# Kernel optimization log

Hardware: AMD Instinct MI355X
Metric: run time of the kernel (lower is better)

## Reference

```python
import jax, jax.numpy as jnp
import numpy as np

N_NODES = 50000
N_EDGES = 400000
IN_DIM = 128
HID_DIM = 128
OUT_DIM = 128


def setup_inputs() -> dict:
    key = jax.random.key(0)
    k_x, k_e, k_w1, k_b1, k_w2, k_b2 = jax.random.split(key, 6)
    x = jax.random.normal(k_x, (N_NODES, IN_DIM), dtype=jnp.float32)
    edge_index = jax.random.randint(k_e, (2, N_EDGES), 0, N_NODES, dtype=jnp.int64)
    # nn.Linear-style params: W is [out, in], kaiming-uniform-ish init
    lim1 = 1.0 / np.sqrt(IN_DIM)
    lim2 = 1.0 / np.sqrt(HID_DIM)
    W1 = jax.random.uniform(k_w1, (HID_DIM, IN_DIM), jnp.float32, -lim1, lim1)
    b1 = jax.random.uniform(k_b1, (HID_DIM,), jnp.float32, -lim1, lim1)
    W2 = jax.random.uniform(k_w2, (OUT_DIM, HID_DIM), jnp.float32, -lim2, lim2)
    b2 = jax.random.uniform(k_b2, (OUT_DIM,), jnp.float32, -lim2, lim2)
    return {"x": x, "edge_index": edge_index, "W1": W1, "b1": b1, "W2": W2, "b2": b2}


def reference(x, edge_index, W1, b1, W2, b2):
    # h = relu(fc1(x));  dropout in eval mode -> identity
    h = jax.nn.relu(x @ W1.T + b1)                      # [N, hid]
    src, dst = edge_index[0], edge_index[1]
    # gather messages from src, scatter-add (mean) into dst
    agg = jax.ops.segment_sum(h[src], dst, num_segments=N_NODES)      # [N, hid]
    deg = jax.ops.segment_sum(jnp.ones_like(dst, dtype=h.dtype), dst,
                              num_segments=N_NODES)                   # [N]
    deg = jnp.maximum(deg, 1.0)
    agg = agg / deg[:, None]
    # residual add + fc2
    return (agg + h) @ W2.T + b2                        # [N, out]
```

## Files before the change

kernel.cpp:

```cpp
#include <hip/hip_runtime.h>

#define N_NODES 50000
#define N_EDGES 400000
#define DIM 128
#define N_SCAN_BLK ((N_NODES + 255) / 256)
#define BUCKET_BLK ((N_EDGES + 255) / 256)
#define FC1_BLK ((N_NODES + 63) / 64)
#define AGG_BLK (N_NODES / 16)

typedef unsigned short u16;
typedef unsigned int   u32;
typedef __bf16 v8bf  __attribute__((ext_vector_type(8)));
typedef float  f32x4 __attribute__((ext_vector_type(4)));
typedef u16    u16x8 __attribute__((ext_vector_type(8)));

union BF8 { u16x8 u; v8bf b; };

__device__ __forceinline__ float bf2f(u16 u) {
    union { u32 i; float f; } v; v.i = ((u32)u) << 16; return v.f;
}
__device__ __forceinline__ u16 f2bf(float f) {
    union { float f; u32 i; } v; v.f = f; u32 u = v.i;
    return (u16)((u + 0x7FFFu + ((u >> 16) & 1u)) >> 16);
}

__global__ __launch_bounds__(256, 3) void count_fc1_kernel(
    const int* __restrict__ esrc, const int* __restrict__ edst,
    int* __restrict__ counts, int* __restrict__ occ,
    const float* __restrict__ x, const float* __restrict__ W1,
    const float* __restrict__ b1, u16* __restrict__ h)
{
    __shared__ u16 xs[64 * 136];
    const int bid = blockIdx.x;

    if (bid < BUCKET_BLK) {
        int e = bid * 256 + threadIdx.x;
        if (e < N_EDGES) {
            int src = esrc[e], dst = edst[e];
            if ((unsigned)src < N_NODES && (unsigned)dst < N_NODES)
                occ[e] = atomicAdd(&counts[dst], 1);
        }
        return;
    }

    const int t = threadIdx.x;
    const int wave = t >> 6, lane = t & 63, quad = lane >> 4, l15 = lane & 15;
    const int ch = wave >> 1, rh = wave & 1;
    const int row0 = (bid - BUCKET_BLK) * 64;

    BF8 barr[4][4];
#pragma unroll
    for (int ct = 0; ct < 4; ++ct)
#pragma unroll
        for (int ks = 0; ks < 4; ++ks) {
            const float* wp = W1 + (size_t)(ch * 64 + ct * 16 + l15) * DIM
                                 + ks * 32 + quad * 8;
            float4 f0 = *(const float4*)wp;
            float4 f1 = *(const float4*)(wp + 4);
            u16x8 p;
            p[0] = f2bf(f0.x); p[1] = f2bf(f0.y); p[2] = f2bf(f0.z); p[3] = f2bf(f0.w);
            p[4] = f2bf(f1.x); p[5] = f2bf(f1.y); p[6] = f2bf(f1.z); p[7] = f2bf(f1.w);
            barr[ct][ks].u = p;
        }

    {
        int srow = t >> 2, k0 = (t & 3) * 32;
        int grow = row0 + srow; if (grow >= N_NODES) grow = N_NODES - 1;
        const float* xp = x + (size_t)grow * DIM + k0;
#pragma unroll
        for (int j = 0; j < 4; ++j) {
            float4 f0 = *(const float4*)(xp + j * 8);
            float4 f1 = *(const float4*)(xp + j * 8 + 4);
            u16x8 p;
            p[0] = f2bf(f0.x); p[1] = f2bf(f0.y); p[2] = f2bf(f0.z); p[3] = f2bf(f0.w);
            p[4] = f2bf(f1.x); p[5] = f2bf(f1.y); p[6] = f2bf(f1.z); p[7] = f2bf(f1.w);
            *(u16x8*)&xs[srow * 136 + k0 + j * 8] = p;
        }
    }

    f32x4 acc[2][4];
#pragma unroll
    for (int ct = 0; ct < 4; ++ct) {
        float bv = b1[ch * 64 + ct * 16 + l15];
        acc[0][ct] = (f32x4){bv, bv, bv, bv};
        acc[1][ct] = (f32x4){bv, bv, bv, bv};
    }
    __syncthreads();

#pragma unroll
    for (int ks = 0; ks < 4; ++ks) {
        BF8 a0, a1;
        a0.u = *(const u16x8*)&xs[(rh * 32 +  0 + l15) * 136 + ks * 32 + quad * 8];
        a1.u = *(const u16x8*)&xs[(rh * 32 + 16 + l15) * 136 + ks * 32 + quad * 8];
#pragma unroll
        for (int ct = 0; ct < 4; ++ct) {
            acc[0][ct] = __builtin_amdgcn_mfma_f32_16x16x32_bf16(
                a0.b, barr[ct][ks].b, acc[0][ct], 0, 0, 0);
            acc[1][ct] = __builtin_amdgcn_mfma_f32_16x16x32_bf16(
                a1.b, barr[ct][ks].b, acc[1][ct], 0, 0, 0);
        }
    }

#pragma unroll
    for (int rt = 0; rt < 2; ++rt)
#pragma unroll
        for (int i = 0; i < 4; ++i) {
            int row = row0 + rh * 32 + rt * 16 + quad * 4 + i;
            if (row < N_NODES) {
#pragma unroll
                for (int ct = 0; ct < 4; ++ct) {
                    int col = ch * 64 + ct * 16 + l15;
                    h[(size_t)row * DIM + col] = f2bf(fmaxf(acc[rt][ct][i], 0.f));
                }
            }
        }
}

__global__ __launch_bounds__(256) void scan_ticket_kernel(
    const int* __restrict__ counts, int* __restrict__ row_ptr,
    int* __restrict__ gcursor)
{
    __shared__ int tmp[256];
    __shared__ int sbase;
    const int t = threadIdx.x;
    const int i = blockIdx.x * 256 + t;
    int v = (i < N_NODES) ? counts[i] : 0;
    tmp[t] = v;
    __syncthreads();
#pragma unroll
    for (int ofs = 1; ofs < 256; ofs <<= 1) {
        int add = (t >= ofs) ? tmp[t - ofs] : 0;
        __syncthreads();
        tmp[t] += add;
        __syncthreads();
    }
    if (t == 255) sbase = atomicAdd(gcursor, tmp[255]);
    __syncthreads();
    if (i < N_NODES) row_ptr[i] = sbase + tmp[t] - v;
}

__global__ __launch_bounds__(256) void scatter_kernel(
    const int* __restrict__ esrc, const int* __restrict__ edst,
    const int* __restrict__ occ, const int* __restrict__ row_ptr,
    int* __restrict__ esorted)
{
    int e = blockIdx.x * 256 + threadIdx.x;
    if (e >= N_EDGES) return;
    int src = esrc[e], dst = edst[e];
    if ((unsigned)src < N_NODES && (unsigned)dst < N_NODES)
        esorted[row_ptr[dst] + occ[e]] = src;
}

__global__ __launch_bounds__(256) void agg_fc2_kernel(
    const int* __restrict__ row_ptr, const int* __restrict__ counts,
    const int* __restrict__ esorted, const u16* __restrict__ h,
    const float* __restrict__ W2, const float* __restrict__ b2,
    float* __restrict__ out)
{
    __shared__ u16 xs[16 * 136];
    const int t = threadIdx.x;
    const int wv = t >> 6, lane = t & 63, quad = lane >> 4, l15 = lane & 15;
    const int row0 = blockIdx.x * 16;

    {
        const int s = wv * 4 + quad;
        const int n = row0 + s;
        const int start = row_ptr[n];
        const int deg   = counts[n];
        const int end   = start + deg;

        u16x8 hres = *(const u16x8*)(h + (size_t)n * DIM + l15 * 8);

        float a[8];
#pragma unroll
        for (int j = 0; j < 8; ++j) a[j] = 0.f;

        int e = start;
        for (; e + 8 <= end; e += 8) {
            int s0 = esorted[e + 0], s1 = esorted[e + 1];
            int s2 = esorted[e + 2], s3 = esorted[e + 3];
            int s4 = esorted[e + 4], s5 = esorted[e + 5];
            int s6 = esorted[e + 6], s7 = esorted[e + 7];
            u16x8 v0 = *(const u16x8*)(h + (size_t)s0 * DIM + l15 * 8);
            u16x8 v1 = *(const u16x8*)(h + (size_t)s1 * DIM + l15 * 8);
            u16x8 v2 = *(const u16x8*)(h + (size_t)s2 * DIM + l15 * 8);
            u16x8 v3 = *(const u16x8*)(h + (size_t)s3 * DIM + l15 * 8);
            u16x8 v4 = *(const u16x8*)(h + (size_t)s4 * DIM + l15 * 8);
            u16x8 v5 = *(const u16x8*)(h + (size_t)s5 * DIM + l15 * 8);
            u16x8 v6 = *(const u16x8*)(h + (size_t)s6 * DIM + l15 * 8);
            u16x8 v7 = *(const u16x8*)(h + (size_t)s7 * DIM + l15 * 8);
#pragma unroll
            for (int j = 0; j < 8; ++j) {
                a[j] += bf2f(v0[j]); a[j] += bf2f(v1[j]);
                a[j] += bf2f(v2[j]); a[j] += bf2f(v3[j]);
                a[j] += bf2f(v4[j]); a[j] += bf2f(v5[j]);
                a[j] += bf2f(v6[j]); a[j] += bf2f(v7[j]);
            }
        }
        for (; e + 4 <= end; e += 4) {
            int s0 = esorted[e + 0], s1 = esorted[e + 1];
            int s2 = esorted[e + 2], s3 = esorted[e + 3];
            u16x8 v0 = *(const u16x8*)(h + (size_t)s0 * DIM + l15 * 8);
            u16x8 v1 = *(const u16x8*)(h + (size_t)s1 * DIM + l15 * 8);
            u16x8 v2 = *(const u16x8*)(h + (size_t)s2 * DIM + l15 * 8);
            u16x8 v3 = *(const u16x8*)(h + (size_t)s3 * DIM + l15 * 8);
#pragma unroll
            for (int j = 0; j < 8; ++j) {
                a[j] += bf2f(v0[j]); a[j] += bf2f(v1[j]);
                a[j] += bf2f(v2[j]); a[j] += bf2f(v3[j]);
            }
        }
        for (; e < end; ++e) {
            u16x8 v = *(const u16x8*)(h + (size_t)esorted[e] * DIM + l15 * 8);
#pragma unroll
            for (int j = 0; j < 8; ++j) a[j] += bf2f(v[j]);
        }

        float inv = (deg > 0) ? 1.f / (float)deg : 1.f;
        u16x8 pk;
#pragma unroll
        for (int j = 0; j < 8; ++j)
            pk[j] = f2bf(a[j] * inv + bf2f(hres[j]));
        *(u16x8*)&xs[s * 136 + l15 * 8] = pk;
    }

    BF8 barr[2][4];
#pragma unroll
    for (int ct = 0; ct < 2; ++ct)
#pragma unroll
        for (int ks = 0; ks < 4; ++ks) {
            const float* wp = W2 + (size_t)(wv * 32 + ct * 16 + l15) * DIM
                                 + ks * 32 + quad * 8;
            float4 f0 = *(const float4*)wp;
            float4 f1 = *(const float4*)(wp + 4);
            u16x8 p;
            p[0] = f2bf(f0.x); p[1] = f2bf(f0.y); p[2] = f2bf(f0.z); p[3] = f2bf(f0.w);
            p[4] = f2bf(f1.x); p[5] = f2bf(f1.y); p[6] = f2bf(f1.z); p[7] = f2bf(f1.w);
            barr[ct][ks].u = p;
        }

    f32x4 acc[2];
#pragma unroll
    for (int ct = 0; ct < 2; ++ct) {
        float bv = b2[wv * 32 + ct * 16 + l15];
        acc[ct] = (f32x4){bv, bv, bv, bv};
    }
    __syncthreads();

#pragma unroll
    for (int ks = 0; ks < 4; ++ks) {
        BF8 a0;
        a0.u = *(const u16x8*)&xs[l15 * 136 + ks * 32 + quad * 8];
#pragma unroll
        for (int ct = 0; ct < 2; ++ct) {
            acc[ct] = __builtin_amdgcn_mfma_f32_16x16x32_bf16(
                a0.b, barr[ct][ks].b, acc[ct], 0, 0, 0);
        }
    }

#pragma unroll
    for (int i = 0; i < 4; ++i) {
        int row = row0 + quad * 4 + i;
#pragma unroll
        for (int ct = 0; ct < 2; ++ct) {
            int col = wv * 32 + ct * 16 + l15;
            out[(size_t)row * DIM + col] = acc[ct][i];
        }
    }
}

extern "C" void kernel_launch(void* const* d_in, const int* in_sizes, int n_in,
                              void* d_out, int out_size, void* d_ws, size_t ws_size,
                              hipStream_t stream)
{
    const float* x  = (const float*)d_in[0];
    const int*   ei = (const int*)d_in[1];
    const float* W1 = (const float*)d_in[2];
    const float* b1 = (const float*)d_in[3];
    const float* W2 = (const float*)d_in[4];
    const float* b2 = (const float*)d_in[5];
    float* out = (float*)d_out;

    const int* esrc = ei;
    const int* edst = ei + N_EDGES;

    char* ws = (char*)d_ws;
    size_t off = 0;
    u16* h       = (u16*)(ws + off); off += (size_t)N_NODES * DIM * 2;
    int* counts  = (int*)(ws + off); off += (size_t)N_NODES * 4;
    int* gcursor = (int*)(ws + off); off += 4;
    int* row_ptr = (int*)(ws + off); off += (size_t)N_NODES * 4;
    int* occ     = (int*)(ws + off); off += (size_t)N_EDGES * 4;
    int* esorted = (int*)(ws + off); off += (size_t)N_EDGES * 4;

    hipMemsetAsync(counts, 0, (size_t)(N_NODES + 1) * 4, stream);

    count_fc1_kernel<<<BUCKET_BLK + FC1_BLK, 256, 0, stream>>>(
        esrc, edst, counts, occ, x, W1, b1, h);
    scan_ticket_kernel<<<N_SCAN_BLK, 256, 0, stream>>>(
        counts, row_ptr, gcursor);
    scatter_kernel<<<BUCKET_BLK, 256, 0, stream>>>(
        esrc, edst, occ, row_ptr, esorted);
    agg_fc2_kernel<<<AGG_BLK, 256, 0, stream>>>(
        row_ptr, counts, esorted, h, W2, b2, out);
}
```

Before: 175.7 us.

## Pad CSR rows to multiples of four, vectorize edge kernels, precast W2

The scan rounds each node's degree up to a multiple of four and fills the padding slots with a sentinel index that points to a zeroed extra row of h. The aggregation loop can then read neighbor indices as int4 with no scalar tail. The count and scatter kernels each handle four edges per thread using int4 loads. W2 is converted to bf16 once inside the first kernel, so agg blocks no longer reconvert it. The edge bounds checks are dropped, and the padding adds extra gathers of the zero row plus more esorted storage.

New measurement: 161.2 us. 8.2% less time.

```diff
diff --git a/kernel.cpp b/kernel.cpp
--- a/kernel.cpp
+++ b/kernel.cpp
@@ -4,9 +4,10 @@
 #define N_EDGES 400000
 #define DIM 128
 #define N_SCAN_BLK ((N_NODES + 255) / 256)
-#define BUCKET_BLK ((N_EDGES + 255) / 256)
+#define CNT_BLK ((N_EDGES + 1023) / 1024)
 #define FC1_BLK ((N_NODES + 63) / 64)
 #define AGG_BLK (N_NODES / 16)
+#define PADDED_E (N_EDGES + 3 * N_NODES)
 
 typedef unsigned short u16;
 typedef unsigned int   u32;
@@ -24,29 +25,44 @@
     return (u16)((u + 0x7FFFu + ((u >> 16) & 1u)) >> 16);
 }
 
-__global__ __launch_bounds__(256, 3) void count_fc1_kernel(
+__global__ __launch_bounds__(256, 3) void count_cast_fc1_kernel(
     const int* __restrict__ esrc, const int* __restrict__ edst,
     int* __restrict__ counts, int* __restrict__ occ,
+    const float* __restrict__ W2, u16* __restrict__ Wb2,
     const float* __restrict__ x, const float* __restrict__ W1,
     const float* __restrict__ b1, u16* __restrict__ h)
 {
     __shared__ u16 xs[64 * 136];
     const int bid = blockIdx.x;
 
-    if (bid < BUCKET_BLK) {
-        int e = bid * 256 + threadIdx.x;
-        if (e < N_EDGES) {
-            int src = esrc[e], dst = edst[e];
-            if ((unsigned)src < N_NODES && (unsigned)dst < N_NODES)
-                occ[e] = atomicAdd(&counts[dst], 1);
-        }
+    if (bid < CNT_BLK) {
+        int e0 = bid * 1024 + threadIdx.x * 4;
+        if (e0 < N_EDGES) {
+            int4 d4 = *(const int4*)(edst + e0);
+            int4 o;
+            o.x = atomicAdd(&counts[d4.x], 1);
+            o.y = atomicAdd(&counts[d4.y], 1);
+            o.z = atomicAdd(&counts[d4.z], 1);
+            o.w = atomicAdd(&counts[d4.w], 1);
+            *(int4*)(occ + e0) = o;
+        }
+        return;
+    }
+    if (bid < CNT_BLK + 64) {
+        int i = (bid - CNT_BLK) * 256 + threadIdx.x;
+        Wb2[i] = f2bf(W2[i]);
+        return;
+    }
+    if (bid == CNT_BLK + 64) {
+        if (threadIdx.x < 128)
+            *(u32*)(h + (size_t)N_NODES * DIM + threadIdx.x * 2) = 0u;
         return;
     }
 
     const int t = threadIdx.x;
     const int wave = t >> 6, lane = t & 63, quad = lane >> 4, l15 = lane & 15;
     const int ch = wave >> 1, rh = wave & 1;
-    const int row0 = (bid - BUCKET_BLK) * 64;
+    const int row0 = (bid - (CNT_BLK + 65)) * 64;
 
     BF8 barr[4][4];
 #pragma unroll
@@ -118,14 +134,15 @@
 
 __global__ __launch_bounds__(256) void scan_ticket_kernel(
     const int* __restrict__ counts, int* __restrict__ row_ptr,
-    int* __restrict__ gcursor)
+    int* __restrict__ gcursor, int* __restrict__ esorted)
 {
     __shared__ int tmp[256];
     __shared__ int sbase;
     const int t = threadIdx.x;
     const int i = blockIdx.x * 256 + t;
-    int v = (i < N_NODES) ? counts[i] : 0;
-    tmp[t] = v;
+    int deg = (i < N_NODES) ? counts[i] : 0;
+    int p = (deg + 3) & ~3;
+    tmp[t] = p;
     __syncthreads();
 #pragma unroll
     for (int ofs = 1; ofs < 256; ofs <<= 1) {
@@ -136,7 +153,11 @@
     }
     if (t == 255) sbase = atomicAdd(gcursor, tmp[255]);
     __syncthreads();
-    if (i < N_NODES) row_ptr[i] = sbase + tmp[t] - v;
+    if (i < N_NODES) {
+        int r = sbase + tmp[t] - p;
+        row_ptr[i] = r;
+        for (int k = deg; k < p; ++k) esorted[r + k] = N_NODES;
+    }
 }
 
 __global__ __launch_bounds__(256) void scatter_kernel(
@@ -144,17 +165,21 @@
     const int* __restrict__ occ, const int* __restrict__ row_ptr,
     int* __restrict__ esorted)
 {
-    int e = blockIdx.x * 256 + threadIdx.x;
-    if (e >= N_EDGES) return;
-    int src = esrc[e], dst = edst[e];
-    if ((unsigned)src < N_NODES && (unsigned)dst < N_NODES)
-        esorted[row_ptr[dst] + occ[e]] = src;
+    int e0 = blockIdx.x * 1024 + threadIdx.x * 4;
+    if (e0 >= N_EDGES) return;
+    int4 s4 = *(const int4*)(esrc + e0);
+    int4 d4 = *(const int4*)(edst + e0);
+    int4 o4 = *(const int4*)(occ + e0);
+    esorted[row_ptr[d4.x] + o4.x] = s4.x;
+    esorted[row_ptr[d4.y] + o4.y] = s4.y;
+    esorted[row_ptr[d4.z] + o4.z] = s4.z;
+    esorted[row_ptr[d4.w] + o4.w] = s4.w;
 }
 
 __global__ __launch_bounds__(256) void agg_fc2_kernel(
     const int* __restrict__ row_ptr, const int* __restrict__ counts,
     const int* __restrict__ esorted, const u16* __restrict__ h,
-    const float* __restrict__ W2, const float* __restrict__ b2,
+    const u16* __restrict__ Wb2, const float* __restrict__ b2,
     float* __restrict__ out)
 {
     __shared__ u16 xs[16 * 136];
@@ -167,7 +192,7 @@
         const int n = row0 + s;
         const int start = row_ptr[n];
         const int deg   = counts[n];
-        const int end   = start + deg;
+        const int plen  = (deg + 3) & ~3;
 
         u16x8 hres = *(const u16x8*)(h + (size_t)n * DIM + l15 * 8);
 
@@ -175,20 +200,19 @@
 #pragma unroll
         for (int j = 0; j < 8; ++j) a[j] = 0.f;
 
-        int e = start;
-        for (; e + 8 <= end; e += 8) {
-            int s0 = esorted[e + 0], s1 = esorted[e + 1];
-            int s2 = esorted[e + 2], s3 = esorted[e + 3];
-            int s4 = esorted[e + 4], s5 = esorted[e + 5];
-            int s6 = esorted[e + 6], s7 = esorted[e + 7];
-            u16x8 v0 = *(const u16x8*)(h + (size_t)s0 * DIM + l15 * 8);
-            u16x8 v1 = *(const u16x8*)(h + (size_t)s1 * DIM + l15 * 8);
-            u16x8 v2 = *(const u16x8*)(h + (size_t)s2 * DIM + l15 * 8);
-            u16x8 v3 = *(const u16x8*)(h + (size_t)s3 * DIM + l15 * 8);
-            u16x8 v4 = *(const u16x8*)(h + (size_t)s4 * DIM + l15 * 8);
-            u16x8 v5 = *(const u16x8*)(h + (size_t)s5 * DIM + l15 * 8);
-            u16x8 v6 = *(const u16x8*)(h + (size_t)s6 * DIM + l15 * 8);
-            u16x8 v7 = *(const u16x8*)(h + (size_t)s7 * DIM + l15 * 8);
+        const int* ep = esorted + start;
+        int k = 0;
+        for (; k + 8 <= plen; k += 8) {
+            int4 ia = *(const int4*)(ep + k);
+            int4 ib = *(const int4*)(ep + k + 4);
+            u16x8 v0 = *(const u16x8*)(h + (size_t)ia.x * DIM + l15 * 8);
+            u16x8 v1 = *(const u16x8*)(h + (size_t)ia.y * DIM + l15 * 8);
+            u16x8 v2 = *(const u16x8*)(h + (size_t)ia.z * DIM + l15 * 8);
+            u16x8 v3 = *(const u16x8*)(h + (size_t)ia.w * DIM + l15 * 8);
+            u16x8 v4 = *(const u16x8*)(h + (size_t)ib.x * DIM + l15 * 8);
+            u16x8 v5 = *(const u16x8*)(h + (size_t)ib.y * DIM + l15 * 8);
+            u16x8 v6 = *(const u16x8*)(h + (size_t)ib.z * DIM + l15 * 8);
+            u16x8 v7 = *(const u16x8*)(h + (size_t)ib.w * DIM + l15 * 8);
 #pragma unroll
             for (int j = 0; j < 8; ++j) {
                 a[j] += bf2f(v0[j]); a[j] += bf2f(v1[j]);
@@ -197,24 +221,18 @@
                 a[j] += bf2f(v6[j]); a[j] += bf2f(v7[j]);
             }
         }
-        for (; e + 4 <= end; e += 4) {
-            int s0 = esorted[e + 0], s1 = esorted[e + 1];
-            int s2 = esorted[e + 2], s3 = esorted[e + 3];
-            u16x8 v0 = *(const u16x8*)(h + (size_t)s0 * DIM + l15 * 8);
-            u16x8 v1 = *(const u16x8*)(h + (size_t)s1 * DIM + l15 * 8);
-            u16x8 v2 = *(const u16x8*)(h + (size_t)s2 * DIM + l15 * 8);
-            u16x8 v3 = *(const u16x8*)(h + (size_t)s3 * DIM + l15 * 8);
+        if (k < plen) {
+            int4 ia = *(const int4*)(ep + k);
+            u16x8 v0 = *(const u16x8*)(h + (size_t)ia.x * DIM + l15 * 8);
+            u16x8 v1 = *(const u16x8*)(h + (size_t)ia.y * DIM + l15 * 8);
+            u16x8 v2 = *(const u16x8*)(h + (size_t)ia.z * DIM + l15 * 8);
+            u16x8 v3 = *(const u16x8*)(h + (size_t)ia.w * DIM + l15 * 8);
 #pragma unroll
             for (int j = 0; j < 8; ++j) {
                 a[j] += bf2f(v0[j]); a[j] += bf2f(v1[j]);
                 a[j] += bf2f(v2[j]); a[j] += bf2f(v3[j]);
             }
         }
-        for (; e < end; ++e) {
-            u16x8 v = *(const u16x8*)(h + (size_t)esorted[e] * DIM + l15 * 8);
-#pragma unroll
-            for (int j = 0; j < 8; ++j) a[j] += bf2f(v[j]);
-        }
 
         float inv = (deg > 0) ? 1.f / (float)deg : 1.f;
         u16x8 pk;
@@ -228,16 +246,9 @@
 #pragma unroll
     for (int ct = 0; ct < 2; ++ct)
 #pragma unroll
-        for (int ks = 0; ks < 4; ++ks) {
-            const float* wp = W2 + (size_t)(wv * 32 + ct * 16 + l15) * DIM
-                                 + ks * 32 + quad * 8;
-            float4 f0 = *(const float4*)wp;
-            float4 f1 = *(const float4*)(wp + 4);
-            u16x8 p;
-            p[0] = f2bf(f0.x); p[1] = f2bf(f0.y); p[2] = f2bf(f0.z); p[3] = f2bf(f0.w);
-            p[4] = f2bf(f1.x); p[5] = f2bf(f1.y); p[6] = f2bf(f1.z); p[7] = f2bf(f1.w);
-            barr[ct][ks].u = p;
-        }
+        for (int ks = 0; ks < 4; ++ks)
+            barr[ct][ks].u = *(const u16x8*)(
+                Wb2 + (size_t)(wv * 32 + ct * 16 + l15) * DIM + ks * 32 + quad * 8);
 
     f32x4 acc[2];
 #pragma unroll
@@ -286,21 +297,22 @@
 
     char* ws = (char*)d_ws;
     size_t off = 0;
-    u16* h       = (u16*)(ws + off); off += (size_t)N_NODES * DIM * 2;
+    u16* h       = (u16*)(ws + off); off += (size_t)(N_NODES + 1) * DIM * 2;
+    u16* Wb2     = (u16*)(ws + off); off += (size_t)DIM * DIM * 2;
     int* counts  = (int*)(ws + off); off += (size_t)N_NODES * 4;
     int* gcursor = (int*)(ws + off); off += 4;
     int* row_ptr = (int*)(ws + off); off += (size_t)N_NODES * 4;
     int* occ     = (int*)(ws + off); off += (size_t)N_EDGES * 4;
-    int* esorted = (int*)(ws + off); off += (size_t)N_EDGES * 4;
+    int* esorted = (int*)(ws + off); off += (size_t)PADDED_E * 4;
 
     hipMemsetAsync(counts, 0, (size_t)(N_NODES + 1) * 4, stream);
 
-    count_fc1_kernel<<<BUCKET_BLK + FC1_BLK, 256, 0, stream>>>(
-        esrc, edst, counts, occ, x, W1, b1, h);
+    count_cast_fc1_kernel<<<CNT_BLK + 65 + FC1_BLK, 256, 0, stream>>>(
+        esrc, edst, counts, occ, W2, Wb2, x, W1, b1, h);
     scan_ticket_kernel<<<N_SCAN_BLK, 256, 0, stream>>>(
-        counts, row_ptr, gcursor);
-    scatter_kernel<<<BUCKET_BLK, 256, 0, stream>>>(
+        counts, row_ptr, gcursor, esorted);
+    scatter_kernel<<<CNT_BLK, 256, 0, stream>>>(
         esrc, edst, occ, row_ptr, esorted);
     agg_fc2_kernel<<<AGG_BLK, 256, 0, stream>>>(
-        row_ptr, counts, esorted, h, W2, b2, out);
-}
+        row_ptr, counts, esorted, h, Wb2, b2, out);
+}
```
